# Performance work log

Hardware: AMD Instinct MI355X
Metric: run time of the kernel (lower is better)

## Reference

```python
import jax, jax.numpy as jnp
import numpy as np

N_NODES = 50000
N_RAND_EDGES = 800000
IN_FEATS = 128
NUM_HEADS = 4
OUT_FEATS = 32
NEG_SLOPE = 0.2


def setup_inputs() -> dict:
    key = jax.random.key(0)
    k_feat, k_src, k_dst, k_w, k_al, k_ar, k_b = jax.random.split(key, 7)
    feat = jax.random.normal(k_feat, (N_NODES, IN_FEATS), dtype=jnp.float32)
    # random edges + self-loops so every node has in-degree >= 1 (DGL requirement)
    src_r = jax.random.randint(k_src, (N_RAND_EDGES,), 0, N_NODES)
    dst_r = jax.random.randint(k_dst, (N_RAND_EDGES,), 0, N_NODES)
    loops = jnp.arange(N_NODES, dtype=src_r.dtype)
    src = jnp.concatenate([src_r, loops]).astype(jnp.int64)
    dst = jnp.concatenate([dst_r, loops]).astype(jnp.int64)
    W = jax.random.normal(k_w, (NUM_HEADS * OUT_FEATS, IN_FEATS), dtype=jnp.float32) * 0.05
    attn_l = jax.random.normal(k_al, (1, NUM_HEADS, OUT_FEATS), dtype=jnp.float32) * 0.1
    attn_r = jax.random.normal(k_ar, (1, NUM_HEADS, OUT_FEATS), dtype=jnp.float32) * 0.1
    bias = jnp.zeros((NUM_HEADS * OUT_FEATS,), dtype=jnp.float32)
    return {"feat": feat, "src": src, "dst": dst, "W": W,
            "attn_l": attn_l, "attn_r": attn_r, "bias": bias}


def _gat_forward(feat, src, dst, W, attn_l, attn_r, bias):
    n = feat.shape[0]
    # shared projection: in homogeneous path feat_src2 = feat_dst2 = fc(h)
    ft = (feat @ W.T).reshape(n, NUM_HEADS, OUT_FEATS)       # [N,H,D]
    el = jnp.sum(ft * attn_l, axis=-1)                        # [N,H]
    er = jnp.sum(ft * attn_r, axis=-1)                        # [N,H]
    e = el[src] + er[dst]                                     # [E,H]
    e = jnp.where(e > 0, e, NEG_SLOPE * e)                    # leaky_relu
    # edge softmax per destination node (numerically stable)
    m = jax.ops.segment_max(e, dst, num_segments=n)           # [N,H]
    ex = jnp.exp(e - m[dst])
    s = jax.ops.segment_sum(ex, dst, num_segments=n)          # [N,H]
    a = ex / s[dst]                                           # [E,H]
    # u_mul_e -> sum : attention-weighted aggregation
    msg1 = ft[src] * a[:, :, None]                            # [E,H,D]
    initial_ft = jax.ops.segment_sum(msg1, dst, num_segments=n)
    # u_mul_v -> sum : elementwise src*dst product aggregation
    msg2 = ft[src] * ft[dst]                                  # [E,H,D]
    add_ft = jax.ops.segment_sum(msg2, dst, num_segments=n)
    rst = initial_ft + add_ft + bias.reshape(1, NUM_HEADS, OUT_FEATS)
    return rst


def reference(feat, src, dst, W, attn_l, attn_r, bias):
    return _gat_forward(feat, src, dst, W, attn_l, attn_r, bias)
```

## Files before the change

### kernel.cpp

```cpp
#include <hip/hip_runtime.h>
#include <hip/hip_bf16.h>

#define IN_FEATS 128
#define HD 128
#define NEG_SLOPE 0.2f
#define LDR 128
#define CAP 64
#define BINW 256
#define CAPB 5120
#define NBLK 256
#define GM 64
#define LDA 136

typedef short s8v __attribute__((ext_vector_type(8)));
typedef float f4v __attribute__((ext_vector_type(4)));
typedef float f2v __attribute__((ext_vector_type(2)));

static __device__ __forceinline__ unsigned short f2bf(float f) {
    unsigned int u = __float_as_uint(f);
    unsigned int r = (u + 0x7FFFu + ((u >> 16) & 1u)) >> 16;
    return (unsigned short)r;
}
static __device__ __forceinline__ float bf2f(unsigned short h) {
    return __uint_as_float(((unsigned int)h) << 16);
}

static __device__ __forceinline__ void stage_W(unsigned short (*Wb)[LDA],
                                               const float* __restrict__ W) {
    const float4* W4 = (const float4*)W;
    for (int i = threadIdx.x; i < 4096; i += 256) {
        int r = i >> 5, q = i & 31;
        float4 w = W4[i];
        ushort4 o;
        o.x = f2bf(w.x); o.y = f2bf(w.y); o.z = f2bf(w.z); o.w = f2bf(w.w);
        *(ushort4*)&Wb[r][q * 4] = o;
    }
}

static __device__ __forceinline__ void gemm_tile(
        unsigned short (*Wb)[LDA], unsigned short (*Ab)[LDA],
        const float* __restrict__ feat, const float* __restrict__ attn_l,
        const float* __restrict__ attn_r, unsigned short* __restrict__ ftb,
        float* __restrict__ el, float* __restrict__ er, int N, int rbase) {
    const int tid  = threadIdx.x;
    const int wave = tid >> 6;
    const int lane = tid & 63;
    const int m    = lane & 15;
    const int quad = lane >> 4;

    const float4* F4 = (const float4*)feat;
    for (int i = tid; i < 2048; i += 256) {
        int r = i >> 5, q = i & 31;
        int gr = rbase + r;
        float4 v = (gr < N) ? F4[(size_t)gr * 32 + q]
                            : make_float4(0.f, 0.f, 0.f, 0.f);
        ushort4 o;
        o.x = f2bf(v.x); o.y = f2bf(v.y); o.z = f2bf(v.z); o.w = f2bf(v.w);
        *(ushort4*)&Ab[r][q * 4] = o;
    }
    __syncthreads();

    f4v acc[8];
#pragma unroll
    for (int t = 0; t < 8; ++t) acc[t] = (f4v){0.f, 0.f, 0.f, 0.f};

    const int arow = wave * 16 + m;
#pragma unroll
    for (int k0 = 0; k0 < 4; ++k0) {
        s8v a = *(const s8v*)&Ab[arow][k0 * 32 + quad * 8];
#pragma unroll
        for (int t = 0; t < 8; ++t) {
            s8v b = *(const s8v*)&Wb[t * 16 + m][k0 * 32 + quad * 8];
            acc[t] = __builtin_amdgcn_mfma_f32_16x16x32_bf16(a, b, acc[t], 0, 0, 0);
        }
    }

#pragma unroll
    for (int reg = 0; reg < 4; ++reg) {
        int gr = rbase + wave * 16 + quad * 4 + reg;
        if (gr < N) {
            unsigned short* dstrow = &ftb[(size_t)gr * LDR];
#pragma unroll
            for (int t = 0; t < 8; ++t)
                dstrow[t * 16 + m] = f2bf(acc[t][reg]);
        }
    }

    float al[8], ar[8];
#pragma unroll
    for (int t = 0; t < 8; ++t) {
        al[t] = attn_l[t * 16 + m];
        ar[t] = attn_r[t * 16 + m];
    }
#pragma unroll
    for (int h = 0; h < 4; ++h) {
#pragma unroll
        for (int reg = 0; reg < 4; ++reg) {
            float pl = acc[2 * h][reg] * al[2 * h] + acc[2 * h + 1][reg] * al[2 * h + 1];
            float pr = acc[2 * h][reg] * ar[2 * h] + acc[2 * h + 1][reg] * ar[2 * h + 1];
            pl += __shfl_xor(pl, 1); pr += __shfl_xor(pr, 1);
            pl += __shfl_xor(pl, 2); pr += __shfl_xor(pr, 2);
            pl += __shfl_xor(pl, 4); pr += __shfl_xor(pr, 4);
            pl += __shfl_xor(pl, 8); pr += __shfl_xor(pr, 8);
            if (m == 0) {
                int gr = rbase + wave * 16 + quad * 4 + reg;
                if (gr < N) {
                    el[gr * 4 + h] = pl;
                    er[gr * 4 + h] = pr;
                }
            }
        }
    }
}

__global__ __launch_bounds__(256) void count_gemm(
        const float* __restrict__ feat, const float* __restrict__ W,
        const float* __restrict__ attn_l, const float* __restrict__ attn_r,
        const int* __restrict__ dst, int E, int* __restrict__ cntBB,
        unsigned short* __restrict__ ftb, float* __restrict__ el,
        float* __restrict__ er, int N, int nbins) {
    __shared__ __align__(16) char smem[52224];
    const int tid = threadIdx.x;
    if (blockIdx.x < NBLK) {
        int* hist = (int*)smem;
        hist[tid] = 0;
        __syncthreads();
        const int chunk = (E + NBLK - 1) / NBLK;
        const int base = blockIdx.x * chunk;
        const int end = min(base + chunk, E);
        for (int i = base + tid; i < end; i += 256)
            atomicAdd(&hist[dst[i] >> 8], 1);
        __syncthreads();
        cntBB[blockIdx.x * 256 + tid] = hist[tid];
        return;
    }
    unsigned short (*Wb)[LDA] = (unsigned short (*)[LDA])smem;
    unsigned short (*Ab)[LDA] = (unsigned short (*)[LDA])(smem + 128 * LDA * 2);
    stage_W(Wb, W);
    gemm_tile(Wb, Ab, feat, attn_l, attn_r, ftb, el, er, N,
              (blockIdx.x - NBLK) * GM);
}

__global__ __launch_bounds__(256) void scan_scatter(
        const int* __restrict__ src, const int* __restrict__ dst, int E,
        const int* __restrict__ cntBB, unsigned int* __restrict__ binbuf,
        int nbins) {
    __shared__ int obase[256];
    __shared__ int lcnt[256];
    const int tid = threadIdx.x;
    const int bid = blockIdx.x;
    {
        int acc0 = 0, acc1 = 0, acc2 = 0, acc3 = 0;
        int acc4 = 0, acc5 = 0, acc6 = 0, acc7 = 0;
        int b = 0;
        for (; b + 8 <= bid; b += 8) {
            acc0 += cntBB[(b + 0) * 256 + tid];
            acc1 += cntBB[(b + 1) * 256 + tid];
            acc2 += cntBB[(b + 2) * 256 + tid];
            acc3 += cntBB[(b + 3) * 256 + tid];
            acc4 += cntBB[(b + 4) * 256 + tid];
            acc5 += cntBB[(b + 5) * 256 + tid];
            acc6 += cntBB[(b + 6) * 256 + tid];
            acc7 += cntBB[(b + 7) * 256 + tid];
        }
        for (; b < bid; ++b) acc0 += cntBB[b * 256 + tid];
        obase[tid] = ((acc0 + acc1) + (acc2 + acc3)) + ((acc4 + acc5) + (acc6 + acc7));
    }
    lcnt[tid] = 0;
    __syncthreads();
    const int chunk = (E + NBLK - 1) / NBLK;
    const int base = bid * chunk;
    const int end = min(base + chunk, E);
    for (int i = base + tid; i < end; i += 256) {
        int d = dst[i];
        int s = src[i];
        int bin = d >> 8;
        int r = atomicAdd(&lcnt[bin], 1);
        int idx = obase[bin] + r;
        if (idx < CAPB)
            binbuf[(size_t)bin * CAPB + idx] =
                ((unsigned int)(d & 255) << 16) | (unsigned int)s;
    }
}

__global__ __launch_bounds__(256) void bucket_build(
        const unsigned int* __restrict__ binbuf, const int* __restrict__ cntBB,
        int* __restrict__ cnt, unsigned short* __restrict__ bucket, int N) {
    __shared__ int lcnt[256];
    __shared__ int red[256];
    const int bin = blockIdx.x;
    const int tid = threadIdx.x;
    lcnt[tid] = 0;
    red[tid] = cntBB[tid * 256 + bin];
    __syncthreads();
    for (int s = 128; s > 0; s >>= 1) {
        if (tid < s) red[tid] += red[tid + s];
        __syncthreads();
    }
    const int total = min(red[0], CAPB);
    const unsigned int* bb = binbuf + (size_t)bin * CAPB;
    for (int i = tid; i < total; i += 256) {
        unsigned int v = bb[i];
        int dl = (int)(v >> 16);
        unsigned short s = (unsigned short)(v & 0xFFFFu);
        int pos = atomicAdd(&lcnt[dl], 1);
        if (pos < CAP)
            bucket[(((size_t)(bin << 8) + dl) << 6) + pos] = s;
    }
    __syncthreads();
    int gn = (bin << 8) + tid;
    if (gn < N) cnt[gn] = lcnt[tid];
}

__global__ __launch_bounds__(256) void aggregate_kernel(
        const unsigned short* __restrict__ ftb, const float* __restrict__ el,
        const float* __restrict__ er, const int* __restrict__ cnt,
        const unsigned short* __restrict__ bucket, const float* __restrict__ bias,
        float* __restrict__ out, int N) {
    const int n    = (blockIdx.x * blockDim.x + threadIdx.x) >> 6;
    const int lane = threadIdx.x & 63;
    if (n >= N) return;
    const int h  = lane >> 4;
    const int c0 = lane * 2;

    const float ern = er[(n << 2) + h];
    unsigned int tn = *(const unsigned int*)(ftb + ((size_t)n << 7) + c0);
    f2v ftn; ftn.x = __uint_as_float(tn << 16);
    ftn.y = __uint_as_float(tn & 0xFFFF0000u);

    int deg = min(cnt[n], CAP);
    const unsigned short* eb = bucket + ((size_t)n << 6);

    f2v accA = (f2v){0.f, 0.f};
    f2v accB = (f2v){0.f, 0.f};
    float sum = 0.f;

    int i = 0;
    for (; i + 4 <= deg; i += 4) {
        ushort4 s4 = *(const ushort4*)&eb[i];
        int sA = s4.x, sB = s4.y, sC = s4.z, sD = s4.w;
        float eA = el[(sA << 2) + h];
        float eB = el[(sB << 2) + h];
        float eC = el[(sC << 2) + h];
        float eD = el[(sD << 2) + h];
        unsigned int fA = *(const unsigned int*)(ftb + ((size_t)sA << 7) + c0);
        unsigned int fB = *(const unsigned int*)(ftb + ((size_t)sB << 7) + c0);
        unsigned int fC = *(const unsigned int*)(ftb + ((size_t)sC << 7) + c0);
        unsigned int fD = *(const unsigned int*)(ftb + ((size_t)sD << 7) + c0);
        eA += ern; eB += ern; eC += ern; eD += ern;
        eA = fmaxf(eA, NEG_SLOPE * eA);
        eB = fmaxf(eB, NEG_SLOPE * eB);
        eC = fmaxf(eC, NEG_SLOPE * eC);
        eD = fmaxf(eD, NEG_SLOPE * eD);
        float xA = __expf(eA), xB = __expf(eB);
        float xC = __expf(eC), xD = __expf(eD);
        f2v ffA; ffA.x = __uint_as_float(fA << 16); ffA.y = __uint_as_float(fA & 0xFFFF0000u);
        f2v ffB; ffB.x = __uint_as_float(fB << 16); ffB.y = __uint_as_float(fB & 0xFFFF0000u);
        f2v ffC; ffC.x = __uint_as_float(fC << 16); ffC.y = __uint_as_float(fC & 0xFFFF0000u);
        f2v ffD; ffD.x = __uint_as_float(fD << 16); ffD.y = __uint_as_float(fD & 0xFFFF0000u);
        sum += (xA + xB) + (xC + xD);
        accA += xA * ffA;
        accA += xB * ffB;
        accA += xC * ffC;
        accA += xD * ffD;
        accB += ffA + ffB;
        accB += ffC + ffD;
    }
    for (; i < deg; ++i) {
        int s = eb[i];
        float e = el[(s << 2) + h] + ern;
        e = fmaxf(e, NEG_SLOPE * e);
        float x = __expf(e);
        unsigned int f = *(const unsigned int*)(ftb + ((size_t)s << 7) + c0);
        f2v ff; ff.x = __uint_as_float(f << 16); ff.y = __uint_as_float(f & 0xFFFF0000u);
        sum += x;
        accA += x * ff;
        accB += ff;
    }

    float inv = 1.f / sum;
    f2v o = accA * inv + ftn * accB;
    float2 ov;
    ov.x = o.x + bias[c0];
    ov.y = o.y + bias[c0 + 1];
    *(float2*)(out + (size_t)n * HD + c0) = ov;
}

extern "C" void kernel_launch(void* const* d_in, const int* in_sizes, int n_in,
                              void* d_out, int out_size, void* d_ws, size_t ws_size,
                              hipStream_t stream) {
    const float* feat   = (const float*)d_in[0];
    const int*   src    = (const int*)d_in[1];
    const int*   dst    = (const int*)d_in[2];
    const float* W      = (const float*)d_in[3];
    const float* attn_l = (const float*)d_in[4];
    const float* attn_r = (const float*)d_in[5];
    const float* bias   = (const float*)d_in[6];

    const int N = in_sizes[0] / IN_FEATS;
    const int E = in_sizes[1];
    const int nbins = (N + BINW - 1) / BINW;

    char* p = (char*)d_ws;
    auto alloc = [&](size_t bytes) {
        char* q = p;
        p += (bytes + 255) & ~(size_t)255;
        return q;
    };
    unsigned short* ftb   = (unsigned short*)alloc((size_t)N * LDR * 2);
    float* el       = (float*)alloc((size_t)N * 4 * 4);
    float* er       = (float*)alloc((size_t)N * 4 * 4);
    int*   cnt      = (int*)alloc((size_t)N * 4);
    unsigned short* bucket = (unsigned short*)alloc((size_t)N * CAP * 2);
    unsigned int* binbuf = (unsigned int*)alloc((size_t)nbins * CAPB * 4);
    int*   cntBB    = (int*)alloc((size_t)NBLK * 256 * 4);

    const int gemm_blocks = (N + GM - 1) / GM;
    count_gemm<<<NBLK + gemm_blocks, 256, 0, stream>>>(
        feat, W, attn_l, attn_r, dst, E, cntBB, ftb, el, er, N, nbins);

    scan_scatter<<<NBLK, 256, 0, stream>>>(src, dst, E, cntBB, binbuf, nbins);

    bucket_build<<<nbins, 256, 0, stream>>>(binbuf, cntBB, cnt, bucket, N);

    long long threads = (long long)N * 64;
    int agg_blocks = (int)((threads + 255) / 256);
    aggregate_kernel<<<agg_blocks, 256, 0, stream>>>(ftb, el, er, cnt, bucket,
                                                     bias, (float*)d_out, N);
}
```

Before: 174.2 us.

## Fuse histogram, scatter and bucket build into one kernel with grid barriers

The count, scan/scatter and bucket-build kernels are merged into a single launch alongside the GEMM tiles. Their phases are separated by a software grid barrier built on global atomic counters, which are zeroed with a memset before each launch. This removes two kernel launches and their inter-kernel gaps. In exchange it depends on all 256 build blocks being co-resident, which is not guaranteed since they share the grid with the GEMM blocks. It also adds spin-wait cost and a timeout escape that could silently produce wrong results if it fires.

```diff
diff --git a/kernel.cpp b/kernel.cpp
--- a/kernel.cpp
+++ b/kernel.cpp
@@ -8,7 +8,7 @@
 #define CAP 64
 #define BINW 256
 #define CAPB 5120
-#define NBLK 256
+#define GNB 256
 #define GM 64
 #define LDA 136
 
@@ -23,6 +23,21 @@
 }
 static __device__ __forceinline__ float bf2f(unsigned short h) {
     return __uint_as_float(((unsigned int)h) << 16);
+}
+
+static __device__ __forceinline__ void gbar(unsigned int* ctr, unsigned int target) {
+    __threadfence();
+    __syncthreads();
+    if (threadIdx.x == 0) {
+        __hip_atomic_fetch_add(ctr, 1u, __ATOMIC_ACQ_REL, __HIP_MEMORY_SCOPE_AGENT);
+        long long spins = 0;
+        while (__hip_atomic_load(ctr, __ATOMIC_ACQUIRE, __HIP_MEMORY_SCOPE_AGENT) < target) {
+            __builtin_amdgcn_s_sleep(8);
+            if (++spins > (1LL << 22)) break;
+        }
+    }
+    __syncthreads();
+    __threadfence();
 }
 
 static __device__ __forceinline__ void stage_W(unsigned short (*Wb)[LDA],
@@ -113,43 +128,45 @@
     }
 }
 
-__global__ __launch_bounds__(256) void count_gemm(
+__global__ __launch_bounds__(256) void build_gemm(
         const float* __restrict__ feat, const float* __restrict__ W,
         const float* __restrict__ attn_l, const float* __restrict__ attn_r,
-        const int* __restrict__ dst, int E, int* __restrict__ cntBB,
+        const int* __restrict__ src, const int* __restrict__ dst, int E,
+        int* __restrict__ cntBB, unsigned int* __restrict__ binbuf,
+        int* __restrict__ cnt, unsigned short* __restrict__ bucket,
         unsigned short* __restrict__ ftb, float* __restrict__ el,
-        float* __restrict__ er, int N, int nbins) {
+        float* __restrict__ er, int N, int nbins, unsigned int* __restrict__ bar) {
     __shared__ __align__(16) char smem[52224];
     const int tid = threadIdx.x;
-    if (blockIdx.x < NBLK) {
+    const int bid = blockIdx.x;
+
+    if (bid >= GNB) {
+        unsigned short (*Wb)[LDA] = (unsigned short (*)[LDA])smem;
+        unsigned short (*Ab)[LDA] = (unsigned short (*)[LDA])(smem + 128 * LDA * 2);
+        stage_W(Wb, W);
+        gemm_tile(Wb, Ab, feat, attn_l, attn_r, ftb, el, er, N,
+                  (bid - GNB) * GM);
+        return;
+    }
+
+    const int chunk = (E + GNB - 1) / GNB;
+    const int base  = bid * chunk;
+    const int end   = min(base + chunk, E);
+
+    {
         int* hist = (int*)smem;
         hist[tid] = 0;
         __syncthreads();
-        const int chunk = (E + NBLK - 1) / NBLK;
-        const int base = blockIdx.x * chunk;
-        const int end = min(base + chunk, E);
         for (int i = base + tid; i < end; i += 256)
             atomicAdd(&hist[dst[i] >> 8], 1);
         __syncthreads();
-        cntBB[blockIdx.x * 256 + tid] = hist[tid];
-        return;
-    }
-    unsigned short (*Wb)[LDA] = (unsigned short (*)[LDA])smem;
-    unsigned short (*Ab)[LDA] = (unsigned short (*)[LDA])(smem + 128 * LDA * 2);
-    stage_W(Wb, W);
-    gemm_tile(Wb, Ab, feat, attn_l, attn_r, ftb, el, er, N,
-              (blockIdx.x - NBLK) * GM);
-}
-
-__global__ __launch_bounds__(256) void scan_scatter(
-        const int* __restrict__ src, const int* __restrict__ dst, int E,
-        const int* __restrict__ cntBB, unsigned int* __restrict__ binbuf,
-        int nbins) {
-    __shared__ int obase[256];
-    __shared__ int lcnt[256];
-    const int tid = threadIdx.x;
-    const int bid = blockIdx.x;
+        cntBB[bid * 256 + tid] = hist[tid];
+    }
+    gbar(&bar[0], GNB);
+
     {
+        int* obase = (int*)smem;
+        int* lcnt  = ((int*)smem) + 256;
         int acc0 = 0, acc1 = 0, acc2 = 0, acc3 = 0;
         int acc4 = 0, acc5 = 0, acc6 = 0, acc7 = 0;
         int b = 0;
@@ -165,51 +182,45 @@
         }
         for (; b < bid; ++b) acc0 += cntBB[b * 256 + tid];
         obase[tid] = ((acc0 + acc1) + (acc2 + acc3)) + ((acc4 + acc5) + (acc6 + acc7));
-    }
-    lcnt[tid] = 0;
-    __syncthreads();
-    const int chunk = (E + NBLK - 1) / NBLK;
-    const int base = bid * chunk;
-    const int end = min(base + chunk, E);
-    for (int i = base + tid; i < end; i += 256) {
-        int d = dst[i];
-        int s = src[i];
-        int bin = d >> 8;
-        int r = atomicAdd(&lcnt[bin], 1);
-        int idx = obase[bin] + r;
-        if (idx < CAPB)
-            binbuf[(size_t)bin * CAPB + idx] =
-                ((unsigned int)(d & 255) << 16) | (unsigned int)s;
-    }
-}
-
-__global__ __launch_bounds__(256) void bucket_build(
-        const unsigned int* __restrict__ binbuf, const int* __restrict__ cntBB,
-        int* __restrict__ cnt, unsigned short* __restrict__ bucket, int N) {
-    __shared__ int lcnt[256];
-    __shared__ int red[256];
-    const int bin = blockIdx.x;
-    const int tid = threadIdx.x;
-    lcnt[tid] = 0;
-    red[tid] = cntBB[tid * 256 + bin];
-    __syncthreads();
-    for (int s = 128; s > 0; s >>= 1) {
-        if (tid < s) red[tid] += red[tid + s];
-        __syncthreads();
-    }
-    const int total = min(red[0], CAPB);
-    const unsigned int* bb = binbuf + (size_t)bin * CAPB;
-    for (int i = tid; i < total; i += 256) {
-        unsigned int v = bb[i];
-        int dl = (int)(v >> 16);
-        unsigned short s = (unsigned short)(v & 0xFFFFu);
-        int pos = atomicAdd(&lcnt[dl], 1);
-        if (pos < CAP)
-            bucket[(((size_t)(bin << 8) + dl) << 6) + pos] = s;
-    }
-    __syncthreads();
-    int gn = (bin << 8) + tid;
-    if (gn < N) cnt[gn] = lcnt[tid];
+        lcnt[tid] = 0;
+        __syncthreads();
+        for (int i = base + tid; i < end; i += 256) {
+            int d = dst[i];
+            int s = src[i];
+            int bin = d >> 8;
+            int r = atomicAdd(&lcnt[bin], 1);
+            int idx = obase[bin] + r;
+            if (idx < CAPB)
+                binbuf[(size_t)bin * CAPB + idx] =
+                    ((unsigned int)(d & 255) << 16) | (unsigned int)s;
+        }
+    }
+    gbar(&bar[1], GNB);
+
+    if (bid < nbins) {
+        int* lcnt = (int*)smem;
+        int* red  = ((int*)smem) + 256;
+        lcnt[tid] = 0;
+        red[tid] = cntBB[tid * 256 + bid];
+        __syncthreads();
+        for (int s = 128; s > 0; s >>= 1) {
+            if (tid < s) red[tid] += red[tid + s];
+            __syncthreads();
+        }
+        const int total = min(red[0], CAPB);
+        const unsigned int* bb = binbuf + (size_t)bid * CAPB;
+        for (int i = tid; i < total; i += 256) {
+            unsigned int v = bb[i];
+            int dl = (int)(v >> 16);
+            unsigned short s = (unsigned short)(v & 0xFFFFu);
+            int pos = atomicAdd(&lcnt[dl], 1);
+            if (pos < CAP)
+                bucket[(((size_t)(bid << 8) + dl) << 6) + pos] = s;
+        }
+        __syncthreads();
+        int gn = (bid << 8) + tid;
+        if (gn < N) cnt[gn] = lcnt[tid];
+    }
 }
 
 __global__ __launch_bounds__(256) void aggregate_kernel(
@@ -313,15 +324,15 @@
     int*   cnt      = (int*)alloc((size_t)N * 4);
     unsigned short* bucket = (unsigned short*)alloc((size_t)N * CAP * 2);
     unsigned int* binbuf = (unsigned int*)alloc((size_t)nbins * CAPB * 4);
-    int*   cntBB    = (int*)alloc((size_t)NBLK * 256 * 4);
+    int*   cntBB    = (int*)alloc((size_t)GNB * 256 * 4);
+    unsigned int* bar = (unsigned int*)alloc(256);
+
+    hipMemsetAsync(bar, 0, 2 * sizeof(unsigned int), stream);
 
     const int gemm_blocks = (N + GM - 1) / GM;
-    count_gemm<<<NBLK + gemm_blocks, 256, 0, stream>>>(
-        feat, W, attn_l, attn_r, dst, E, cntBB, ftb, el, er, N, nbins);
-
-    scan_scatter<<<NBLK, 256, 0, stream>>>(src, dst, E, cntBB, binbuf, nbins);
-
-    bucket_build<<<nbins, 256, 0, stream>>>(binbuf, cntBB, cnt, bucket, N);
+    build_gemm<<<GNB + gemm_blocks, 256, 0, stream>>>(
+        feat, W, attn_l, attn_r, src, dst, E, cntBB, binbuf, cnt, bucket,
+        ftb, el, er, N, nbins, bar);
 
     long long threads = (long long)N * 64;
     int agg_blocks = (int)((threads + 255) / 256);
```

Result: slower. 322.8 us (+85.3%).

## Fuse bucket build into aggregation using per-block LDS edge lists

Applied to the files above, without the earlier changes.

Merges the bucket_build and aggregate kernels into one kernel. Each block takes a 32-node slice of a 256-node bin, filters that bin's edges into shared-memory per-node lists, then aggregates its nodes from LDS. This drops one launch and the global bucket/cnt write and read-back. In exchange, every bin's edge buffer is read 8 times (once per group), and each block has 4 waves covering 32 nodes serially, which may reduce parallelism and latency hiding.

```diff
diff --git a/kernel.cpp b/kernel.cpp
--- a/kernel.cpp
+++ b/kernel.cpp
@@ -9,6 +9,8 @@
 #define BINW 256
 #define CAPB 5120
 #define NBLK 256
+#define GPB 8
+#define NPG 32
 #define GM 64
 #define LDA 136
 
@@ -183,14 +185,20 @@
     }
 }
 
-__global__ __launch_bounds__(256) void bucket_build(
+__global__ __launch_bounds__(256) void bucket_agg(
         const unsigned int* __restrict__ binbuf, const int* __restrict__ cntBB,
-        int* __restrict__ cnt, unsigned short* __restrict__ bucket, int N) {
-    __shared__ int lcnt[256];
+        const unsigned short* __restrict__ ftb, const float* __restrict__ el,
+        const float* __restrict__ er, const float* __restrict__ bias,
+        float* __restrict__ out, int N, int nbins) {
+    const int bin = blockIdx.x >> 3;
+    const int g   = blockIdx.x & (GPB - 1);
+    const int tid = threadIdx.x;
+
+    __shared__ unsigned short lb[NPG * CAP];
+    __shared__ int lcnt[NPG];
     __shared__ int red[256];
-    const int bin = blockIdx.x;
-    const int tid = threadIdx.x;
-    lcnt[tid] = 0;
+
+    if (tid < NPG) lcnt[tid] = 0;
     red[tid] = cntBB[tid * 256 + bin];
     __syncthreads();
     for (int s = 128; s > 0; s >>= 1) {
@@ -198,92 +206,90 @@
         __syncthreads();
     }
     const int total = min(red[0], CAPB);
+
     const unsigned int* bb = binbuf + (size_t)bin * CAPB;
     for (int i = tid; i < total; i += 256) {
         unsigned int v = bb[i];
         int dl = (int)(v >> 16);
-        unsigned short s = (unsigned short)(v & 0xFFFFu);
-        int pos = atomicAdd(&lcnt[dl], 1);
-        if (pos < CAP)
-            bucket[(((size_t)(bin << 8) + dl) << 6) + pos] = s;
+        if ((dl >> 5) == g) {
+            int ln = dl & (NPG - 1);
+            int pos = atomicAdd(&lcnt[ln], 1);
+            if (pos < CAP) lb[(ln << 6) + pos] = (unsigned short)(v & 0xFFFFu);
+        }
     }
     __syncthreads();
-    int gn = (bin << 8) + tid;
-    if (gn < N) cnt[gn] = lcnt[tid];
-}
-
-__global__ __launch_bounds__(256) void aggregate_kernel(
-        const unsigned short* __restrict__ ftb, const float* __restrict__ el,
-        const float* __restrict__ er, const int* __restrict__ cnt,
-        const unsigned short* __restrict__ bucket, const float* __restrict__ bias,
-        float* __restrict__ out, int N) {
-    const int n    = (blockIdx.x * blockDim.x + threadIdx.x) >> 6;
-    const int lane = threadIdx.x & 63;
-    if (n >= N) return;
+
+    const int wave = tid >> 6;
+    const int lane = tid & 63;
     const int h  = lane >> 4;
     const int c0 = lane * 2;
 
-    const float ern = er[(n << 2) + h];
-    unsigned int tn = *(const unsigned int*)(ftb + ((size_t)n << 7) + c0);
-    f2v ftn; ftn.x = __uint_as_float(tn << 16);
-    ftn.y = __uint_as_float(tn & 0xFFFF0000u);
-
-    int deg = min(cnt[n], CAP);
-    const unsigned short* eb = bucket + ((size_t)n << 6);
-
-    f2v accA = (f2v){0.f, 0.f};
-    f2v accB = (f2v){0.f, 0.f};
-    float sum = 0.f;
-
-    int i = 0;
-    for (; i + 4 <= deg; i += 4) {
-        ushort4 s4 = *(const ushort4*)&eb[i];
-        int sA = s4.x, sB = s4.y, sC = s4.z, sD = s4.w;
-        float eA = el[(sA << 2) + h];
-        float eB = el[(sB << 2) + h];
-        float eC = el[(sC << 2) + h];
-        float eD = el[(sD << 2) + h];
-        unsigned int fA = *(const unsigned int*)(ftb + ((size_t)sA << 7) + c0);
-        unsigned int fB = *(const unsigned int*)(ftb + ((size_t)sB << 7) + c0);
-        unsigned int fC = *(const unsigned int*)(ftb + ((size_t)sC << 7) + c0);
-        unsigned int fD = *(const unsigned int*)(ftb + ((size_t)sD << 7) + c0);
-        eA += ern; eB += ern; eC += ern; eD += ern;
-        eA = fmaxf(eA, NEG_SLOPE * eA);
-        eB = fmaxf(eB, NEG_SLOPE * eB);
-        eC = fmaxf(eC, NEG_SLOPE * eC);
-        eD = fmaxf(eD, NEG_SLOPE * eD);
-        float xA = __expf(eA), xB = __expf(eB);
-        float xC = __expf(eC), xD = __expf(eD);
-        f2v ffA; ffA.x = __uint_as_float(fA << 16); ffA.y = __uint_as_float(fA & 0xFFFF0000u);
-        f2v ffB; ffB.x = __uint_as_float(fB << 16); ffB.y = __uint_as_float(fB & 0xFFFF0000u);
-        f2v ffC; ffC.x = __uint_as_float(fC << 16); ffC.y = __uint_as_float(fC & 0xFFFF0000u);
-        f2v ffD; ffD.x = __uint_as_float(fD << 16); ffD.y = __uint_as_float(fD & 0xFFFF0000u);
-        sum += (xA + xB) + (xC + xD);
-        accA += xA * ffA;
-        accA += xB * ffB;
-        accA += xC * ffC;
-        accA += xD * ffD;
-        accB += ffA + ffB;
-        accB += ffC + ffD;
-    }
-    for (; i < deg; ++i) {
-        int s = eb[i];
-        float e = el[(s << 2) + h] + ern;
-        e = fmaxf(e, NEG_SLOPE * e);
-        float x = __expf(e);
-        unsigned int f = *(const unsigned int*)(ftb + ((size_t)s << 7) + c0);
-        f2v ff; ff.x = __uint_as_float(f << 16); ff.y = __uint_as_float(f & 0xFFFF0000u);
-        sum += x;
-        accA += x * ff;
-        accB += ff;
-    }
-
-    float inv = 1.f / sum;
-    f2v o = accA * inv + ftn * accB;
-    float2 ov;
-    ov.x = o.x + bias[c0];
-    ov.y = o.y + bias[c0 + 1];
-    *(float2*)(out + (size_t)n * HD + c0) = ov;
+    for (int ln = wave; ln < NPG; ln += 4) {
+        const int n = (bin << 8) + (g << 5) + ln;
+        if (n >= N) break;
+
+        const float ern = er[(n << 2) + h];
+        unsigned int tn = *(const unsigned int*)(ftb + ((size_t)n << 7) + c0);
+        f2v ftn; ftn.x = __uint_as_float(tn << 16);
+        ftn.y = __uint_as_float(tn & 0xFFFF0000u);
+
+        const int deg = min(lcnt[ln], CAP);
+        const unsigned short* eb = &lb[ln << 6];
+
+        f2v accA = (f2v){0.f, 0.f};
+        f2v accB = (f2v){0.f, 0.f};
+        float sum = 0.f;
+
+        int i = 0;
+        for (; i + 4 <= deg; i += 4) {
+            ushort4 s4 = *(const ushort4*)&eb[i];
+            int sA = s4.x, sB = s4.y, sC = s4.z, sD = s4.w;
+            float eA = el[(sA << 2) + h];
+            float eB = el[(sB << 2) + h];
+            float eC = el[(sC << 2) + h];
+            float eD = el[(sD << 2) + h];
+            unsigned int fA = *(const unsigned int*)(ftb + ((size_t)sA << 7) + c0);
+            unsigned int fB = *(const unsigned int*)(ftb + ((size_t)sB << 7) + c0);
+            unsigned int fC = *(const unsigned int*)(ftb + ((size_t)sC << 7) + c0);
+            unsigned int fD = *(const unsigned int*)(ftb + ((size_t)sD << 7) + c0);
+            eA += ern; eB += ern; eC += ern; eD += ern;
+            eA = fmaxf(eA, NEG_SLOPE * eA);
+            eB = fmaxf(eB, NEG_SLOPE * eB);
+            eC = fmaxf(eC, NEG_SLOPE * eC);
+            eD = fmaxf(eD, NEG_SLOPE * eD);
+            float xA = __expf(eA), xB = __expf(eB);
+            float xC = __expf(eC), xD = __expf(eD);
+            f2v ffA; ffA.x = __uint_as_float(fA << 16); ffA.y = __uint_as_float(fA & 0xFFFF0000u);
+            f2v ffB; ffB.x = __uint_as_float(fB << 16); ffB.y = __uint_as_float(fB & 0xFFFF0000u);
+            f2v ffC; ffC.x = __uint_as_float(fC << 16); ffC.y = __uint_as_float(fC & 0xFFFF0000u);
+            f2v ffD; ffD.x = __uint_as_float(fD << 16); ffD.y = __uint_as_float(fD & 0xFFFF0000u);
+            sum += (xA + xB) + (xC + xD);
+            accA += xA * ffA;
+            accA += xB * ffB;
+            accA += xC * ffC;
+            accA += xD * ffD;
+            accB += ffA + ffB;
+            accB += ffC + ffD;
+        }
+        for (; i < deg; ++i) {
+            int s = eb[i];
+            float e = el[(s << 2) + h] + ern;
+            e = fmaxf(e, NEG_SLOPE * e);
+            float x = __expf(e);
+            unsigned int f = *(const unsigned int*)(ftb + ((size_t)s << 7) + c0);
+            f2v ff; ff.x = __uint_as_float(f << 16); ff.y = __uint_as_float(f & 0xFFFF0000u);
+            sum += x;
+            accA += x * ff;
+            accB += ff;
+        }
+
+        float inv = 1.f / sum;
+        f2v o = accA * inv + ftn * accB;
+        float2 ov;
+        ov.x = o.x + bias[c0];
+        ov.y = o.y + bias[c0 + 1];
+        *(float2*)(out + (size_t)n * HD + c0) = ov;
+    }
 }
 
 extern "C" void kernel_launch(void* const* d_in, const int* in_sizes, int n_in,
@@ -307,13 +313,11 @@
         p += (bytes + 255) & ~(size_t)255;
         return q;
     };
-    unsigned short* ftb   = (unsigned short*)alloc((size_t)N * LDR * 2);
-    float* el       = (float*)alloc((size_t)N * 4 * 4);
-    float* er       = (float*)alloc((size_t)N * 4 * 4);
-    int*   cnt      = (int*)alloc((size_t)N * 4);
-    unsigned short* bucket = (unsigned short*)alloc((size_t)N * CAP * 2);
+    unsigned short* ftb  = (unsigned short*)alloc((size_t)N * LDR * 2);
+    float* el      = (float*)alloc((size_t)N * 4 * 4);
+    float* er      = (float*)alloc((size_t)N * 4 * 4);
     unsigned int* binbuf = (unsigned int*)alloc((size_t)nbins * CAPB * 4);
-    int*   cntBB    = (int*)alloc((size_t)NBLK * 256 * 4);
+    int*   cntBB   = (int*)alloc((size_t)NBLK * 256 * 4);
 
     const int gemm_blocks = (N + GM - 1) / GM;
     count_gemm<<<NBLK + gemm_blocks, 256, 0, stream>>>(
@@ -321,10 +325,6 @@
 
     scan_scatter<<<NBLK, 256, 0, stream>>>(src, dst, E, cntBB, binbuf, nbins);
 
-    bucket_build<<<nbins, 256, 0, stream>>>(binbuf, cntBB, cnt, bucket, N);
-
-    long long threads = (long long)N * 64;
-    int agg_blocks = (int)((threads + 255) / 256);
-    aggregate_kernel<<<agg_blocks, 256, 0, stream>>>(ftb, el, er, cnt, bucket,
-                                                     bias, (float*)d_out, N);
-}
+    bucket_agg<<<nbins * GPB, 256, 0, stream>>>(binbuf, cntBB, ftb, el, er,
+                                                bias, (float*)d_out, N, nbins);
+}
```

Measured after the change: 168.5 us. 3.2% less time.
